# Performance work log

Hardware: AMD Instinct MI355X
Metric: run time of the kernel (lower is better)

## Reference

```python
import jax, jax.numpy as jnp
import numpy as np

B, S, H, NH = 2, 2048, 1024, 16
HD = H // NH  # 64


def setup_inputs() -> dict:
    key = jax.random.key(0)
    ks = jax.random.split(key, 9)
    w = lambda k: jax.random.normal(k, (H, H), dtype=jnp.float32) * 0.02  # torch Linear weight [out,in]
    b = lambda k: jax.random.normal(k, (H,), dtype=jnp.float32) * 0.02
    return {
        "hidden_states": jax.random.normal(ks[0], (B, S, H), dtype=jnp.float32),
        "Wq": w(ks[1]), "bq": b(ks[2]),
        "Wk": w(ks[3]), "bk": b(ks[4]),
        "Wv": w(ks[5]), "bv": b(ks[6]),
        "Wo": w(ks[7]), "bo": b(ks[8]),
    }


def reference(hidden_states, Wq, bq, Wk, bk, Wv, bv, Wo, bo):
    b, s, h = hidden_states.shape
    nh, hd = NH, h // NH

    def proj(W, bias):
        y = hidden_states @ W.T + bias  # torch Linear: x W^T + b
        return y.reshape(b, s, nh, hd).transpose(0, 2, 1, 3)  # [b, h, s, d]

    q = proj(Wq, bq)
    k = proj(Wk, bk)
    v = proj(Wv, bv)

    scale = jnp.sqrt(jnp.asarray(hd, dtype=q.dtype))
    scores = jnp.einsum("bhqd,bhkd->bhqk", q, k) / scale  # [b, h, s, s]
    pos = jnp.arange(s)
    causal = pos[:, None] < pos[None, :]  # True where masked (key after query)
    scores = jnp.where(causal[None, None], -jnp.inf, scores)
    attn = jax.nn.softmax(scores, axis=-1)
    out = jnp.einsum("bhqk,bhkd->bhqd", attn, v)
    out = out.transpose(0, 2, 1, 3).reshape(b, s, h)
    return out @ Wo.T + bo
```

## Files before the change

kernel.cpp:

```cpp
#include <hip/hip_runtime.h>
#include <stdint.h>

typedef __bf16 bf16;
typedef __attribute__((ext_vector_type(2))) __bf16 bf16x2;
typedef __attribute__((ext_vector_type(4))) __bf16 bf16x4;
typedef __attribute__((ext_vector_type(8))) __bf16 bf16x8;
typedef __attribute__((ext_vector_type(4))) float f32x4;
typedef __attribute__((ext_vector_type(4))) short s16x4;

#define B_  2
#define S_  2048
#define H_  1024
#define NH_ 16
#define HD_ 64
#define ST  72
#define STV 136

__device__ __forceinline__ void glds16(const bf16* g, bf16* l) {
  __builtin_amdgcn_global_load_lds(
      (const __attribute__((address_space(1))) uint32_t*)g,
      (__attribute__((address_space(3))) uint32_t*)l, 16, 0, 0);
}

__device__ __forceinline__ f32x4 pv_mfma(bf16x4 a, bf16x4 b, f32x4 c) {
#if __has_builtin(__builtin_amdgcn_mfma_f32_16x16x16bf16_1k)
  union U { bf16x4 h; s16x4 s; };
  U ua; ua.h = a;
  U ub; ub.h = b;
  return __builtin_amdgcn_mfma_f32_16x16x16bf16_1k(ua.s, ub.s, c, 0, 0, 0);
#else
  f32x4 d;
  asm volatile("v_mfma_f32_16x16x16_bf16 %0, %1, %2, %3\n\ts_nop 7\n\ts_nop 7"
               : "=v"(d) : "v"(a), "v"(b), "v"(c));
  return d;
#endif
}

__global__ __launch_bounds__(256) void cvt_f32_bf16(
    const float* __restrict__ s0, bf16* __restrict__ d0, int n0,
    const float* __restrict__ s1, bf16* __restrict__ d1,
    const float* __restrict__ s2, bf16* __restrict__ d2,
    const float* __restrict__ s3, bf16* __restrict__ d3,
    const float* __restrict__ s4, bf16* __restrict__ d4, int nw)
{
  const float* s; bf16* d; int n;
  switch (blockIdx.y) {
    case 0:  s = s0; d = d0; n = n0; break;
    case 1:  s = s1; d = d1; n = nw; break;
    case 2:  s = s2; d = d2; n = nw; break;
    case 3:  s = s3; d = d3; n = nw; break;
    default: s = s4; d = d4; n = nw; break;
  }
  const int i = (blockIdx.x * 256 + threadIdx.x) * 8;
  if (i >= n) return;
  float4 v0 = *(const float4*)(s + i);
  float4 v1 = *(const float4*)(s + i + 4);
  bf16x8 o;
  o[0] = (bf16)v0.x; o[1] = (bf16)v0.y; o[2] = (bf16)v0.z; o[3] = (bf16)v0.w;
  o[4] = (bf16)v1.x; o[5] = (bf16)v1.y; o[6] = (bf16)v1.z; o[7] = (bf16)v1.w;
  *(bf16x8*)(d + i) = o;
}

template <typename TY>
__global__ __launch_bounds__(256) void gemm_bt_bias(
    const bf16* __restrict__ X,
    const bf16* __restrict__ W0, const bf16* __restrict__ W1, const bf16* __restrict__ W2,
    const float* __restrict__ b0, const float* __restrict__ b1, const float* __restrict__ b2,
    TY* __restrict__ Y0, TY* __restrict__ Y1, TY* __restrict__ Y2,
    int M, int N, int K)
{
  const bf16* W; const float* bias; TY* Y;
  if (blockIdx.z == 0)      { W = W0; bias = b0; Y = Y0; }
  else if (blockIdx.z == 1) { W = W1; bias = b1; Y = Y1; }
  else                      { W = W2; bias = b2; Y = Y2; }

  __shared__ __align__(16) bf16 As[2][128 * 32];
  __shared__ __align__(16) bf16 Bs[2][128 * 32];

  const int tid  = threadIdx.x;
  const int lane = tid & 63;
  const int wave = tid >> 6;
  const int m0 = blockIdx.y * 128;
  const int n0 = blockIdx.x * 128;
  const int wm = (wave >> 1) * 64;
  const int wn = (wave & 1) * 64;

  const int r0 = tid >> 2,            c0 = (tid & 3) * 8;
  const int r1 = (256 + tid) >> 2,    c1 = ((256 + tid) & 3) * 8;
  const int cb0 = (wave * 64) * 8;
  const int cb1 = (256 + wave * 64) * 8;

  f32x4 acc[4][4] = {};

  glds16(X + (size_t)(m0 + r0) * K + c0, &As[0][cb0]);
  glds16(W + (size_t)(n0 + r0) * K + c0, &Bs[0][cb0]);
  glds16(X + (size_t)(m0 + r1) * K + c1, &As[0][cb1]);
  glds16(W + (size_t)(n0 + r1) * K + c1, &Bs[0][cb1]);

  int pb = 0;
  for (int k0 = 0; k0 < K; k0 += 32, pb ^= 1) {
    __syncthreads();

    if (k0 + 32 < K) {
      const int kn = k0 + 32;
      glds16(X + (size_t)(m0 + r0) * K + kn + c0, &As[pb ^ 1][cb0]);
      glds16(W + (size_t)(n0 + r0) * K + kn + c0, &Bs[pb ^ 1][cb0]);
      glds16(X + (size_t)(m0 + r1) * K + kn + c1, &As[pb ^ 1][cb1]);
      glds16(W + (size_t)(n0 + r1) * K + kn + c1, &Bs[pb ^ 1][cb1]);
    }

    bf16x8 a[4], b[4];
#pragma unroll
    for (int i = 0; i < 4; ++i)
      a[i] = *(const bf16x8*)&As[pb][(wm + i * 16 + (lane & 15)) * 32 + (lane >> 4) * 8];
#pragma unroll
    for (int i = 0; i < 4; ++i)
      b[i] = *(const bf16x8*)&Bs[pb][(wn + i * 16 + (lane & 15)) * 32 + (lane >> 4) * 8];
#pragma unroll
    for (int mi = 0; mi < 4; ++mi)
#pragma unroll
      for (int ni = 0; ni < 4; ++ni)
        acc[mi][ni] = __builtin_amdgcn_mfma_f32_16x16x32_bf16(a[mi], b[ni], acc[mi][ni], 0, 0, 0);
  }

#pragma unroll
  for (int mi = 0; mi < 4; ++mi) {
    const int row = m0 + wm + mi * 16 + (lane >> 4) * 4;
#pragma unroll
    for (int ni = 0; ni < 4; ++ni) {
      const int col = n0 + wn + ni * 16 + (lane & 15);
      const float bv = bias[col];
#pragma unroll
      for (int r = 0; r < 4; ++r)
        Y[(size_t)(row + r) * N + col] = (TY)(acc[mi][ni][r] + bv);
    }
  }
}

__global__ __launch_bounds__(256, 4) void attn_causal(
    const bf16* __restrict__ Q, const bf16* __restrict__ K,
    const bf16* __restrict__ V, bf16* __restrict__ O)
{
  const int qt = blockIdx.x;
  const int bh = blockIdx.y;
  const int b  = bh >> 4;
  const int h  = bh & 15;

  const int tid  = threadIdx.x;
  const int lane = tid & 63;
  const int wave = tid >> 6;
  const int quad = lane >> 4;
  const int l15  = lane & 15;
  const size_t headoff = (size_t)b * S_ * H_ + (size_t)h * HD_;
  const float SCL = 0.125f * 1.44269504f;

  __shared__ __align__(16) bf16 Ks[128 * ST];
  __shared__ __align__(16) bf16 Vt[64 * STV];

  const int q0   = qt * 64;
  const int qrow = q0 + wave * 16 + l15;

  bf16x8 bq[2];
  bq[0] = *(const bf16x8*)(Q + headoff + (size_t)qrow * H_ + quad * 8);
  bq[1] = *(const bf16x8*)(Q + headoff + (size_t)qrow * H_ + 32 + quad * 8);

  float mr = -1e30f, lr = 0.0f;
  f32x4 oacc[4] = {};

  const int niter = (qt >> 1) + 1;
  for (int it = 0; it < niter; ++it) {
    const int k0 = it * 128;
    __syncthreads();

#pragma unroll
    for (int j = 0; j < 4; ++j) {
      const int c = j * 256 + tid, row = c >> 3, col = (c & 7) * 8;
      *(bf16x8*)&Ks[row * ST + col] =
          *(const bf16x8*)(K + headoff + (size_t)(k0 + row) * H_ + col);
    }
    {
      const int vr = (tid & 63) * 2;
      const int vc = (tid >> 6) * 16;
      bf16x8 a0 = *(const bf16x8*)(V + headoff + (size_t)(k0 + vr) * H_ + vc);
      bf16x8 a1 = *(const bf16x8*)(V + headoff + (size_t)(k0 + vr) * H_ + vc + 8);
      bf16x8 c0 = *(const bf16x8*)(V + headoff + (size_t)(k0 + vr + 1) * H_ + vc);
      bf16x8 c1 = *(const bf16x8*)(V + headoff + (size_t)(k0 + vr + 1) * H_ + vc + 8);
#pragma unroll
      for (int e = 0; e < 8; ++e) {
        bf16x2 p0; p0[0] = a0[e]; p0[1] = c0[e];
        *(bf16x2*)&Vt[(vc + e) * STV + vr] = p0;
        bf16x2 p1; p1[0] = a1[e]; p1[1] = c1[e];
        *(bf16x2*)&Vt[(vc + 8 + e) * STV + vr] = p1;
      }
    }
    __syncthreads();

    f32x4 sacc[8] = {};
    __builtin_amdgcn_s_setprio(1);
#pragma unroll
    for (int ks = 0; ks < 2; ++ks) {
#pragma unroll
      for (int mb = 0; mb < 8; ++mb) {
        bf16x8 ak = *(const bf16x8*)&Ks[(mb * 16 + l15) * ST + ks * 32 + quad * 8];
        sacc[mb] = __builtin_amdgcn_mfma_f32_16x16x32_bf16(ak, bq[ks], sacc[mb], 0, 0, 0);
      }
    }
    __builtin_amdgcn_s_setprio(0);

    if (it == niter - 1) {
#pragma unroll
      for (int mb = 0; mb < 8; ++mb) {
        const int kb = k0 + mb * 16 + quad * 4;
#pragma unroll
        for (int r = 0; r < 4; ++r) {
          const float s = sacc[mb][r] * SCL;
          sacc[mb][r] = (kb + r > qrow) ? -1e30f : s;
        }
      }
    } else {
#pragma unroll
      for (int mb = 0; mb < 8; ++mb)
#pragma unroll
        for (int r = 0; r < 4; ++r)
          sacc[mb][r] = sacc[mb][r] * SCL;
    }

    float mx = -1e30f;
#pragma unroll
    for (int mb = 0; mb < 8; ++mb)
      mx = fmaxf(mx, fmaxf(fmaxf(sacc[mb][0], sacc[mb][1]),
                           fmaxf(sacc[mb][2], sacc[mb][3])));
    mx = fmaxf(mx, __shfl_xor(mx, 16, 64));
    mx = fmaxf(mx, __shfl_xor(mx, 32, 64));
    const float mnew  = fmaxf(mr, mx);
    const float alpha = __builtin_amdgcn_exp2f(mr - mnew);
    mr = mnew;

    float sum = 0.0f;
    bf16x4 pwv[8];
#pragma unroll
    for (int mb = 0; mb < 8; ++mb) {
#pragma unroll
      for (int r = 0; r < 4; ++r) {
        const float p = __builtin_amdgcn_exp2f(sacc[mb][r] - mnew);
        sum += p;
        pwv[mb][r] = (bf16)p;
      }
    }
    sum += __shfl_xor(sum, 16, 64);
    sum += __shfl_xor(sum, 32, 64);
    lr = lr * alpha + sum;
#pragma unroll
    for (int db = 0; db < 4; ++db)
#pragma unroll
      for (int r = 0; r < 4; ++r) oacc[db][r] *= alpha;

    __builtin_amdgcn_s_setprio(1);
#pragma unroll
    for (int mb = 0; mb < 8; ++mb) {
#pragma unroll
      for (int db = 0; db < 4; ++db) {
        bf16x4 av = *(const bf16x4*)&Vt[(db * 16 + l15) * STV + mb * 16 + quad * 4];
        oacc[db] = pv_mfma(av, pwv[mb], oacc[db]);
      }
    }
    __builtin_amdgcn_s_setprio(0);
  }

  const float inv = 1.0f / lr;
#pragma unroll
  for (int db = 0; db < 4; ++db) {
    bf16x4 o;
#pragma unroll
    for (int r = 0; r < 4; ++r) o[r] = (bf16)(oacc[db][r] * inv);
    *(bf16x4*)(O + headoff + (size_t)qrow * H_ + db * 16 + quad * 4) = o;
  }
}

extern "C" void kernel_launch(void* const* d_in, const int* in_sizes, int n_in,
                              void* d_out, int out_size, void* d_ws, size_t ws_size,
                              hipStream_t stream) {
  const float* hs = (const float*)d_in[0];
  const float* Wq = (const float*)d_in[1]; const float* bq = (const float*)d_in[2];
  const float* Wk = (const float*)d_in[3]; const float* bk = (const float*)d_in[4];
  const float* Wv = (const float*)d_in[5]; const float* bv = (const float*)d_in[6];
  const float* Wo = (const float*)d_in[7]; const float* bo = (const float*)d_in[8];
  float* out = (float*)d_out;

  const size_t elems = (size_t)B_ * S_ * H_;
  const size_t wel   = (size_t)H_ * H_;
  bf16* hsb = (bf16*)d_ws;
  bf16* AO  = hsb;
  bf16* Wqb = hsb + elems;
  bf16* Wkb = Wqb + wel;
  bf16* Wvb = Wkb + wel;
  bf16* Wob = Wvb + wel;
  bf16* Qw  = Wob + wel;
  bf16* Kw  = Qw + elems;
  bf16* Vw  = Kw + elems;

  cvt_f32_bf16<<<dim3(2048, 5), dim3(256), 0, stream>>>(
      hs, hsb, (int)elems, Wq, Wqb, Wk, Wkb, Wv, Wvb, Wo, Wob, (int)wel);

  const int M = B_ * S_;
  gemm_bt_bias<bf16><<<dim3(H_ / 128, M / 128, 3), dim3(256), 0, stream>>>(
      hsb, Wqb, Wkb, Wvb, bq, bk, bv, Qw, Kw, Vw, M, H_, H_);

  attn_causal<<<dim3(32, B_ * NH_), dim3(256), 0, stream>>>(Qw, Kw, Vw, AO);

  gemm_bt_bias<float><<<dim3(H_ / 128, M / 128, 1), dim3(256), 0, stream>>>(
      AO, Wob, Wob, Wob, bo, bo, bo, out, out, out, M, H_, H_);
}
```

Baseline: 220.9 us.

## Pair causal query tiles per block, double-buffer K/V via LDS-direct loads

Each attention block now processes two query tiles, a low and its mirrored high tile, so every block does about the same causal work and each K/V tile is staged once and reused by both. K tiles are staged with global_load_lds into a swizzled unpadded layout. K and V are double-buffered so the next tile's loads overlap the current tile's compute. The grid is remapped to 512 linear blocks spread across heads, and launch bounds drop to 2 blocks per CU to fit the doubled LDS and the extra register state. The risk is lower occupancy and register pressure from holding two sets of accumulators.

```diff
diff --git a/kernel.cpp b/kernel.cpp
--- a/kernel.cpp
+++ b/kernel.cpp
@@ -13,7 +13,6 @@
 #define H_  1024
 #define NH_ 16
 #define HD_ 64
-#define ST  72
 #define STV 136
 
 __device__ __forceinline__ void glds16(const bf16* g, bf16* l) {
@@ -137,14 +136,97 @@
   }
 }
 
-__global__ __launch_bounds__(256, 4) void attn_causal(
+
+__device__ __forceinline__ void attn_tile_step(
+    const bf16* Ksb, const bf16* Vtb, const bf16x8 bq[2], int qrow, int k0,
+    bool maskit, float& mr, float& lr, f32x4 oacc[4], int l15, int quad)
+{
+  const float SCL = 0.125f * 1.44269504f;
+
+  f32x4 sacc[8] = {};
+  __builtin_amdgcn_s_setprio(1);
+#pragma unroll
+  for (int ks = 0; ks < 2; ++ks) {
+#pragma unroll
+    for (int mb = 0; mb < 8; ++mb) {
+      const int row = mb * 16 + l15;
+      const int ch  = (ks * 4 + quad) ^ (l15 & 7);
+      bf16x8 ak = *(const bf16x8*)&Ksb[row * 64 + ch * 8];
+      sacc[mb] = __builtin_amdgcn_mfma_f32_16x16x32_bf16(ak, bq[ks], sacc[mb], 0, 0, 0);
+    }
+  }
+  __builtin_amdgcn_s_setprio(0);
+
+  if (maskit) {
+#pragma unroll
+    for (int mb = 0; mb < 8; ++mb) {
+      const int kb = k0 + mb * 16 + quad * 4;
+#pragma unroll
+      for (int r = 0; r < 4; ++r) {
+        const float s = sacc[mb][r] * SCL;
+        sacc[mb][r] = (kb + r > qrow) ? -1e30f : s;
+      }
+    }
+  } else {
+#pragma unroll
+    for (int mb = 0; mb < 8; ++mb)
+#pragma unroll
+      for (int r = 0; r < 4; ++r)
+        sacc[mb][r] = sacc[mb][r] * SCL;
+  }
+
+  float mx = -1e30f;
+#pragma unroll
+  for (int mb = 0; mb < 8; ++mb)
+    mx = fmaxf(mx, fmaxf(fmaxf(sacc[mb][0], sacc[mb][1]),
+                         fmaxf(sacc[mb][2], sacc[mb][3])));
+  mx = fmaxf(mx, __shfl_xor(mx, 16, 64));
+  mx = fmaxf(mx, __shfl_xor(mx, 32, 64));
+  const float mnew  = fmaxf(mr, mx);
+  const float alpha = __builtin_amdgcn_exp2f(mr - mnew);
+  mr = mnew;
+
+  float sum = 0.0f;
+  bf16x4 pwv[8];
+#pragma unroll
+  for (int mb = 0; mb < 8; ++mb) {
+#pragma unroll
+    for (int r = 0; r < 4; ++r) {
+      const float p = __builtin_amdgcn_exp2f(sacc[mb][r] - mnew);
+      sum += p;
+      pwv[mb][r] = (bf16)p;
+    }
+  }
+  sum += __shfl_xor(sum, 16, 64);
+  sum += __shfl_xor(sum, 32, 64);
+  lr = lr * alpha + sum;
+#pragma unroll
+  for (int db = 0; db < 4; ++db)
+#pragma unroll
+    for (int r = 0; r < 4; ++r) oacc[db][r] *= alpha;
+
+  __builtin_amdgcn_s_setprio(1);
+#pragma unroll
+  for (int mb = 0; mb < 8; ++mb) {
+#pragma unroll
+    for (int db = 0; db < 4; ++db) {
+      bf16x4 av = *(const bf16x4*)&Vtb[(db * 16 + l15) * STV + mb * 16 + quad * 4];
+      oacc[db] = pv_mfma(av, pwv[mb], oacc[db]);
+    }
+  }
+  __builtin_amdgcn_s_setprio(0);
+}
+
+__global__ __launch_bounds__(256, 2) void attn_causal(
     const bf16* __restrict__ Q, const bf16* __restrict__ K,
     const bf16* __restrict__ V, bf16* __restrict__ O)
 {
-  const int qt = blockIdx.x;
-  const int bh = blockIdx.y;
-  const int b  = bh >> 4;
-  const int h  = bh & 15;
+  const int lin  = blockIdx.x;
+  const int slot = lin >> 3;
+  const int bh   = (lin & 7) * 4 + (slot >> 4);
+  const int pair = slot & 15;
+  const int b    = bh >> 4;
+  const int h    = bh & 15;
 
   const int tid  = threadIdx.x;
   const int lane = tid & 63;
@@ -152,129 +234,108 @@
   const int quad = lane >> 4;
   const int l15  = lane & 15;
   const size_t headoff = (size_t)b * S_ * H_ + (size_t)h * HD_;
-  const float SCL = 0.125f * 1.44269504f;
-
-  __shared__ __align__(16) bf16 Ks[128 * ST];
-  __shared__ __align__(16) bf16 Vt[64 * STV];
-
-  const int q0   = qt * 64;
-  const int qrow = q0 + wave * 16 + l15;
-
-  bf16x8 bq[2];
-  bq[0] = *(const bf16x8*)(Q + headoff + (size_t)qrow * H_ + quad * 8);
-  bq[1] = *(const bf16x8*)(Q + headoff + (size_t)qrow * H_ + 32 + quad * 8);
-
-  float mr = -1e30f, lr = 0.0f;
-  f32x4 oacc[4] = {};
-
-  const int niter = (qt >> 1) + 1;
-  for (int it = 0; it < niter; ++it) {
-    const int k0 = it * 128;
-    __syncthreads();
-
-#pragma unroll
-    for (int j = 0; j < 4; ++j) {
-      const int c = j * 256 + tid, row = c >> 3, col = (c & 7) * 8;
-      *(bf16x8*)&Ks[row * ST + col] =
-          *(const bf16x8*)(K + headoff + (size_t)(k0 + row) * H_ + col);
-    }
-    {
-      const int vr = (tid & 63) * 2;
-      const int vc = (tid >> 6) * 16;
-      bf16x8 a0 = *(const bf16x8*)(V + headoff + (size_t)(k0 + vr) * H_ + vc);
-      bf16x8 a1 = *(const bf16x8*)(V + headoff + (size_t)(k0 + vr) * H_ + vc + 8);
-      bf16x8 c0 = *(const bf16x8*)(V + headoff + (size_t)(k0 + vr + 1) * H_ + vc);
-      bf16x8 c1 = *(const bf16x8*)(V + headoff + (size_t)(k0 + vr + 1) * H_ + vc + 8);
-#pragma unroll
-      for (int e = 0; e < 8; ++e) {
-        bf16x2 p0; p0[0] = a0[e]; p0[1] = c0[e];
-        *(bf16x2*)&Vt[(vc + e) * STV + vr] = p0;
-        bf16x2 p1; p1[0] = a1[e]; p1[1] = c1[e];
-        *(bf16x2*)&Vt[(vc + 8 + e) * STV + vr] = p1;
-      }
-    }
-    __syncthreads();
-
-    f32x4 sacc[8] = {};
-    __builtin_amdgcn_s_setprio(1);
-#pragma unroll
-    for (int ks = 0; ks < 2; ++ks) {
-#pragma unroll
-      for (int mb = 0; mb < 8; ++mb) {
-        bf16x8 ak = *(const bf16x8*)&Ks[(mb * 16 + l15) * ST + ks * 32 + quad * 8];
-        sacc[mb] = __builtin_amdgcn_mfma_f32_16x16x32_bf16(ak, bq[ks], sacc[mb], 0, 0, 0);
-      }
-    }
-    __builtin_amdgcn_s_setprio(0);
-
-    if (it == niter - 1) {
-#pragma unroll
-      for (int mb = 0; mb < 8; ++mb) {
-        const int kb = k0 + mb * 16 + quad * 4;
-#pragma unroll
-        for (int r = 0; r < 4; ++r) {
-          const float s = sacc[mb][r] * SCL;
-          sacc[mb][r] = (kb + r > qrow) ? -1e30f : s;
-        }
-      }
-    } else {
-#pragma unroll
-      for (int mb = 0; mb < 8; ++mb)
-#pragma unroll
-        for (int r = 0; r < 4; ++r)
-          sacc[mb][r] = sacc[mb][r] * SCL;
-    }
-
-    float mx = -1e30f;
-#pragma unroll
-    for (int mb = 0; mb < 8; ++mb)
-      mx = fmaxf(mx, fmaxf(fmaxf(sacc[mb][0], sacc[mb][1]),
-                           fmaxf(sacc[mb][2], sacc[mb][3])));
-    mx = fmaxf(mx, __shfl_xor(mx, 16, 64));
-    mx = fmaxf(mx, __shfl_xor(mx, 32, 64));
-    const float mnew  = fmaxf(mr, mx);
-    const float alpha = __builtin_amdgcn_exp2f(mr - mnew);
-    mr = mnew;
-
-    float sum = 0.0f;
-    bf16x4 pwv[8];
-#pragma unroll
-    for (int mb = 0; mb < 8; ++mb) {
-#pragma unroll
-      for (int r = 0; r < 4; ++r) {
-        const float p = __builtin_amdgcn_exp2f(sacc[mb][r] - mnew);
-        sum += p;
-        pwv[mb][r] = (bf16)p;
-      }
-    }
-    sum += __shfl_xor(sum, 16, 64);
-    sum += __shfl_xor(sum, 32, 64);
-    lr = lr * alpha + sum;
-#pragma unroll
-    for (int db = 0; db < 4; ++db)
-#pragma unroll
-      for (int r = 0; r < 4; ++r) oacc[db][r] *= alpha;
-
-    __builtin_amdgcn_s_setprio(1);
-#pragma unroll
-    for (int mb = 0; mb < 8; ++mb) {
-#pragma unroll
-      for (int db = 0; db < 4; ++db) {
-        bf16x4 av = *(const bf16x4*)&Vt[(db * 16 + l15) * STV + mb * 16 + quad * 4];
-        oacc[db] = pv_mfma(av, pwv[mb], oacc[db]);
-      }
-    }
-    __builtin_amdgcn_s_setprio(0);
-  }
-
-  const float inv = 1.0f / lr;
+  const bf16* Kp = K + headoff;
+  const bf16* Vp = V + headoff;
+
+  __shared__ __align__(16) bf16 Ks[2][128 * 64];
+  __shared__ __align__(16) bf16 Vt[2][64 * STV];
+
+  const int qlo = pair, qhi = 31 - pair;
+  const int nl  = (qlo >> 1) + 1;
+  const int nh  = (qhi >> 1) + 1;
+  const int qrowL = qlo * 64 + wave * 16 + l15;
+  const int qrowH = qhi * 64 + wave * 16 + l15;
+
+  bf16x8 bqL[2], bqH[2];
+  bqL[0] = *(const bf16x8*)(Q + headoff + (size_t)qrowL * H_ + quad * 8);
+  bqL[1] = *(const bf16x8*)(Q + headoff + (size_t)qrowL * H_ + 32 + quad * 8);
+  bqH[0] = *(const bf16x8*)(Q + headoff + (size_t)qrowH * H_ + quad * 8);
+  bqH[1] = *(const bf16x8*)(Q + headoff + (size_t)qrowH * H_ + 32 + quad * 8);
+
+  const int vr = lane * 2;
+  const int vc = wave * 16;
+
+#define STAGE_K(k0_, buf_)                                                  \
+  {                                                                         \
+    _Pragma("unroll")                                                       \
+    for (int i = 0; i < 4; ++i) {                                           \
+      const int n = i * 256 + tid;                                          \
+      const int row = n >> 3;                                               \
+      const int cg  = (n & 7) ^ (row & 7);                                  \
+      glds16(Kp + (size_t)((k0_) + row) * H_ + cg * 8,                      \
+             &Ks[buf_][(i * 256 + wave * 64) * 8]);                         \
+    }                                                                       \
+  }
+
+#define LOAD_V(k0_)                                                         \
+  {                                                                         \
+    vreg[0] = *(const bf16x8*)(Vp + (size_t)((k0_) + vr) * H_ + vc);        \
+    vreg[1] = *(const bf16x8*)(Vp + (size_t)((k0_) + vr) * H_ + vc + 8);    \
+    vreg[2] = *(const bf16x8*)(Vp + (size_t)((k0_) + vr + 1) * H_ + vc);    \
+    vreg[3] = *(const bf16x8*)(Vp + (size_t)((k0_) + vr + 1) * H_ + vc + 8);\
+  }
+
+#define WRITE_V(buf_)                                                       \
+  {                                                                         \
+    _Pragma("unroll")                                                       \
+    for (int e = 0; e < 8; ++e) {                                           \
+      bf16x2 p0; p0[0] = vreg[0][e]; p0[1] = vreg[2][e];                    \
+      *(bf16x2*)&Vt[buf_][(vc + e) * STV + vr] = p0;                        \
+      bf16x2 p1; p1[0] = vreg[1][e]; p1[1] = vreg[3][e];                    \
+      *(bf16x2*)&Vt[buf_][(vc + 8 + e) * STV + vr] = p1;                    \
+    }                                                                       \
+  }
+
+  bf16x8 vreg[4];
+
+  STAGE_K(0, 0);
+  LOAD_V(0);
+  WRITE_V(0);
+  __syncthreads();
+
+  float mrL = -1e30f, lrL = 0.0f, mrH = -1e30f, lrH = 0.0f;
+  f32x4 oL[4] = {}, oH[4] = {};
+
+  for (int it = 0; it < nh; ++it) {
+    const int c = it & 1;
+    const bool pre = (it + 1 < nh);
+
+    if (pre) {
+      STAGE_K((it + 1) * 128, c ^ 1);
+      LOAD_V((it + 1) * 128);
+    }
+
+    attn_tile_step(Ks[c], Vt[c], bqH, qrowH, it * 128, it == nh - 1,
+                   mrH, lrH, oH, l15, quad);
+    if (it < nl)
+      attn_tile_step(Ks[c], Vt[c], bqL, qrowL, it * 128, it == nl - 1,
+                     mrL, lrL, oL, l15, quad);
+
+    if (pre) {
+      WRITE_V(c ^ 1);
+      __syncthreads();
+    }
+  }
+
+  const float invL = 1.0f / lrL;
 #pragma unroll
   for (int db = 0; db < 4; ++db) {
     bf16x4 o;
 #pragma unroll
-    for (int r = 0; r < 4; ++r) o[r] = (bf16)(oacc[db][r] * inv);
-    *(bf16x4*)(O + headoff + (size_t)qrow * H_ + db * 16 + quad * 4) = o;
-  }
+    for (int r = 0; r < 4; ++r) o[r] = (bf16)(oL[db][r] * invL);
+    *(bf16x4*)(O + headoff + (size_t)qrowL * H_ + db * 16 + quad * 4) = o;
+  }
+  const float invH = 1.0f / lrH;
+#pragma unroll
+  for (int db = 0; db < 4; ++db) {
+    bf16x4 o;
+#pragma unroll
+    for (int r = 0; r < 4; ++r) o[r] = (bf16)(oH[db][r] * invH);
+    *(bf16x4*)(O + headoff + (size_t)qrowH * H_ + db * 16 + quad * 4) = o;
+  }
+#undef STAGE_K
+#undef LOAD_V
+#undef WRITE_V
 }
 
 extern "C" void kernel_launch(void* const* d_in, const int* in_sizes, int n_in,
@@ -306,7 +367,7 @@
   gemm_bt_bias<bf16><<<dim3(H_ / 128, M / 128, 3), dim3(256), 0, stream>>>(
       hsb, Wqb, Wkb, Wvb, bq, bk, bv, Qw, Kw, Vw, M, H_, H_);
 
-  attn_causal<<<dim3(32, B_ * NH_), dim3(256), 0, stream>>>(Qw, Kw, Vw, AO);
+  attn_causal<<<dim3(512), dim3(256), 0, stream>>>(Qw, Kw, Vw, AO);
 
   gemm_bt_bias<float><<<dim3(H_ / 128, M / 128, 1), dim3(256), 0, stream>>>(
       AO, Wob, Wob, Wob, bo, bo, bo, out, out, out, M, H_, H_);
```

Measured after the change: 199.3 us. 9.8% less time.
